# Performance work log

Hardware: AMD Instinct MI355X
Metric: run time of the kernel (lower is better)

## Reference

```python
import jax, jax.numpy as jnp
import numpy as np

N_HOPS = 3
N_NODES = 500000  # n_users + n_items


def setup_inputs() -> dict:
    key = jax.random.key(0)
    k1, k2, k3, k4, k5 = jax.random.split(key, 5)
    n_users, n_items, d, nnz = 100000, 400000, 64, 1250000
    return {
        "user_embed": jax.random.normal(k1, (n_users, d), dtype=jnp.float32),
        "item_embed": jax.random.normal(k2, (n_items, d), dtype=jnp.float32),
        "adj_row": jax.random.randint(k3, (nnz,), 0, n_users + n_items, dtype=jnp.int32),
        "adj_col": jax.random.randint(k4, (nnz,), 0, n_users + n_items, dtype=jnp.int32),
        "adj_val": jax.random.uniform(k5, (nnz,), dtype=jnp.float32),
        "n_users": n_users,
    }


def reference(user_embed, item_embed, adj_row, adj_col, adj_val, n_users):
    # all_embed: [N, d]
    all_embed = jnp.concatenate([user_embed, item_embed], axis=0)

    def spmm(x):
        # sparse @ dense: gather source-node features, scale by edge value,
        # scatter-add into destination rows. COO SpMM == SpecialSpmm.
        msgs = adj_val[:, None] * x[adj_col]          # [nnz, d]
        return jax.ops.segment_sum(msgs, adj_row, num_segments=N_NODES)

    agg = all_embed
    embs = [all_embed]
    for _ in range(N_HOPS):
        agg = spmm(agg)
        embs.append(agg)
    embs = jnp.stack(embs, axis=1)  # [N, n_hops+1, d]
    return embs[:n_users], embs[n_users:]
```

## Files before the change

### kernel.cpp

```cpp
#include <hip/hip_runtime.h>


#define DFEAT 64
#define ELLW 12

typedef float f32x4 __attribute__((ext_vector_type(4)));

__device__ inline unsigned bf16rne(float x) {
    unsigned u = __float_as_uint(x);
    u += 0x7FFF + ((u >> 16) & 1);
    return u;
}
__device__ inline unsigned pack2(float lo, float hi) {
    return (bf16rne(lo) >> 16) | (bf16rne(hi) & 0xFFFF0000u);
}
__device__ inline float bflo(unsigned w) { return __uint_as_float(w << 16); }
__device__ inline float bfhi(unsigned w) { return __uint_as_float(w & 0xFFFF0000u); }

__global__ void gc_zero(int4* __restrict__ p, int n4) {
    int i = blockIdx.x * blockDim.x + threadIdx.x;
    if (i < n4) p[i] = make_int4(0, 0, 0, 0);
}

__global__ void gc_fat(const float4* __restrict__ user4,
                       const float4* __restrict__ item4,
                       float4* __restrict__ out4, uint2* __restrict__ shadow0,
                       const int* __restrict__ row, const int* __restrict__ col,
                       const float* __restrict__ val,
                       int* __restrict__ cnt, float2* __restrict__ ell,
                       int* __restrict__ ovfcnt, int4* __restrict__ ovf,
                       int n_users, int n_nodes, int nnz, int initB) {
    int b = blockIdx.x;
    if (b < initB) {
        int tid = b * blockDim.x + threadIdx.x;
        if (tid >= n_nodes * 16) return;
        int node = tid >> 4;
        int q = tid & 15;
        float4 v = (node < n_users) ? user4[(size_t)node * 16 + q]
                                    : item4[(size_t)(node - n_users) * 16 + q];
        f32x4 nv = {v.x, v.y, v.z, v.w};
        __builtin_nontemporal_store(nv, (f32x4*)(out4 + (size_t)node * 64 + q));
        shadow0[(size_t)node * 16 + q] = make_uint2(pack2(v.x, v.y), pack2(v.z, v.w));
    } else {
        int i = (b - initB) * blockDim.x + threadIdx.x;
        if (i >= nnz) return;
        int r = row[i];
        int pos = atomicAdd(&cnt[r], 1);
        if (pos < ELLW) {
            ell[(size_t)r * ELLW + pos] = make_float2(__int_as_float(col[i] << 3), val[i]);
        } else {
            int o = atomicAdd(ovfcnt, 1);
            ovf[o] = make_int4(r, col[i] << 6, __float_as_int(val[i]), 0);
        }
    }
}

__global__ void gc_hop(const int* __restrict__ cnt,
                       const float4* __restrict__ ell4,
                       const int4* __restrict__ ssrc,
                       int4* __restrict__ sdst,
                       float* __restrict__ out, int hop, int n_nodes) {
    int tid = blockIdx.x * blockDim.x + threadIdx.x;
    int l = tid & 7;
    int r = tid >> 3;
    if (r >= n_nodes) return;
    int c = cnt[r];
    if (c > ELLW) c = ELLW;
    float4 a0 = make_float4(0.f, 0.f, 0.f, 0.f);
    float4 a1 = make_float4(0.f, 0.f, 0.f, 0.f);
    int e = 0;
    for (; e + 2 <= c; e += 2) {
        float4 s = ell4[(size_t)r * (ELLW / 2) + (e >> 1)];
        int i0 = __float_as_int(s.x) + l;
        int i1 = __float_as_int(s.z) + l;
        int4 g0 = ssrc[i0];
        int4 g1 = ssrc[i1];
        float v0 = s.y, v1 = s.w;
        a0.x += v0 * bflo(g0.x); a0.y += v0 * bfhi(g0.x);
        a0.z += v0 * bflo(g0.y); a0.w += v0 * bfhi(g0.y);
        a1.x += v0 * bflo(g0.z); a1.y += v0 * bfhi(g0.z);
        a1.z += v0 * bflo(g0.w); a1.w += v0 * bfhi(g0.w);
        a0.x += v1 * bflo(g1.x); a0.y += v1 * bfhi(g1.x);
        a0.z += v1 * bflo(g1.y); a0.w += v1 * bfhi(g1.y);
        a1.x += v1 * bflo(g1.z); a1.y += v1 * bfhi(g1.z);
        a1.z += v1 * bflo(g1.w); a1.w += v1 * bfhi(g1.w);
    }
    if (e < c) {
        float2 s = ((const float2*)ell4)[(size_t)r * ELLW + e];
        int i0 = __float_as_int(s.x) + l;
        int4 g0 = ssrc[i0];
        float v0 = s.y;
        a0.x += v0 * bflo(g0.x); a0.y += v0 * bfhi(g0.x);
        a0.z += v0 * bflo(g0.y); a0.w += v0 * bfhi(g0.y);
        a1.x += v0 * bflo(g0.z); a1.y += v0 * bfhi(g0.z);
        a1.z += v0 * bflo(g0.w); a1.w += v0 * bfhi(g0.w);
    }
    size_t dq = (size_t)r * 64 + (size_t)hop * 16 + l * 2;
    f32x4 n0 = {a0.x, a0.y, a0.z, a0.w};
    f32x4 n1 = {a1.x, a1.y, a1.z, a1.w};
    __builtin_nontemporal_store(n0, (f32x4*)((float4*)out) + dq);
    __builtin_nontemporal_store(n1, (f32x4*)((float4*)out) + dq + 1);
    if (sdst) {
        sdst[(size_t)r * 8 + l] = make_int4(pack2(a0.x, a0.y), pack2(a0.z, a0.w),
                                            pack2(a1.x, a1.y), pack2(a1.z, a1.w));
    }
}

__global__ void gc_ovf(const int* __restrict__ ovfcnt, const int4* __restrict__ ovf,
                       float* __restrict__ out, int hop) {
    int gtid = blockIdx.x * blockDim.x + threadIdx.x;
    int wave = gtid >> 6;
    int lane = gtid & 63;
    int nw = (gridDim.x * blockDim.x) >> 6;
    int cntv = *ovfcnt;
    size_t src_base = (size_t)(hop - 1) * 64 + lane;
    size_t dst_base = (size_t)hop * 64 + lane;
    for (int e = wave; e < cntv; e += nw) {
        int4 ed = ovf[e];
        float v = __int_as_float(ed.z);
        float x = out[(size_t)ed.y * 4 + src_base];
        unsafeAtomicAdd(&out[(size_t)ed.x * 256 + dst_base], v * x);
    }
}

__global__ void gc_sfix(const int* __restrict__ ovfcnt, const int4* __restrict__ ovf,
                        const float* __restrict__ out, unsigned short* __restrict__ shadow,
                        int hop) {
    int cntv = *ovfcnt;
    for (int i = blockIdx.x; i < cntv; i += gridDim.x) {
        int r = ovf[i].x;
        float x = out[(size_t)r * 256 + (size_t)hop * 64 + threadIdx.x];
        shadow[(size_t)r * 64 + threadIdx.x] = (unsigned short)(bf16rne(x) >> 16);
    }
}

__global__ void gc_init_out_full(const float4* __restrict__ user4,
                                 const float4* __restrict__ item4,
                                 float4* __restrict__ out4,
                                 int n_users, int n_nodes) {
    int tid = blockIdx.x * blockDim.x + threadIdx.x;
    if (tid >= n_nodes * 16) return;
    int node = tid >> 4;
    int q = tid & 15;
    float4 v = (node < n_users) ? user4[(size_t)node * 16 + q]
                                : item4[(size_t)(node - n_users) * 16 + q];
    float4 z = make_float4(0.f, 0.f, 0.f, 0.f);
    float4* p = out4 + (size_t)node * 64 + q;
    p[0] = v; p[16] = z; p[32] = z; p[48] = z;
}

__global__ void gc_spmm_atomic(const int* __restrict__ adj_row,
                               const int* __restrict__ adj_col,
                               const float* __restrict__ adj_val,
                               float* __restrict__ out, int hop, int nnz) {
    long long tid = (long long)blockIdx.x * blockDim.x + threadIdx.x;
    int e = (int)(tid >> 6);
    int j = (int)(tid & 63);
    if (e >= nnz) return;
    int r = adj_row[e];
    int c = adj_col[e];
    float v = adj_val[e];
    float x = out[(size_t)c * 256 + (size_t)(hop - 1) * 64 + j];
    unsafeAtomicAdd(&out[(size_t)r * 256 + (size_t)hop * 64 + j], v * x);
}

extern "C" void kernel_launch(void* const* d_in, const int* in_sizes, int n_in,
                              void* d_out, int out_size, void* d_ws, size_t ws_size,
                              hipStream_t stream) {
    const float* user_embed = (const float*)d_in[0];
    const float* item_embed = (const float*)d_in[1];
    const int*   adj_row    = (const int*)d_in[2];
    const int*   adj_col    = (const int*)d_in[3];
    const float* adj_val    = (const float*)d_in[4];
    const int n_users = in_sizes[0] / DFEAT;
    const int n_items = in_sizes[1] / DFEAT;
    const int n_nodes = n_users + n_items;
    const int nnz     = in_sizes[2];
    float* out = (float*)d_out;
    float4* out4 = (float4*)out;

    const int threads = 256;

    size_t off = 0;
    auto carve = [&](size_t bytes) { size_t o = off; off = (off + bytes + 255) & ~(size_t)255; return o; };
    size_t o_cnt    = carve((size_t)n_nodes * 4);
    size_t o_ovfcnt = carve(256);
    size_t zero_end = off;
    size_t o_ell    = carve((size_t)n_nodes * ELLW * 8);
    size_t o_ovf    = carve((size_t)nnz * 16);
    size_t o_shA    = carve((size_t)n_nodes * DFEAT * 2);
    size_t o_shB    = carve((size_t)n_nodes * DFEAT * 2);
    size_t needed = off;

    if (ws_size < needed) {
        int init_blocks = (n_nodes * 16 + threads - 1) / threads;
        hipLaunchKernelGGL(gc_init_out_full, dim3(init_blocks), dim3(threads), 0, stream,
                           (const float4*)user_embed, (const float4*)item_embed,
                           out4, n_users, n_nodes);
        long long spmm_total = (long long)nnz * 64;
        int spmm_blocks = (int)((spmm_total + threads - 1) / threads);
        for (int h = 1; h <= 3; ++h) {
            hipLaunchKernelGGL(gc_spmm_atomic, dim3(spmm_blocks), dim3(threads), 0, stream,
                               adj_row, adj_col, adj_val, out, h, nnz);
        }
        return;
    }

    char* ws = (char*)d_ws;
    int*    cnt    = (int*)(ws + o_cnt);
    int*    ovfcnt = (int*)(ws + o_ovfcnt);
    float2* ell    = (float2*)(ws + o_ell);
    int4*   ovf    = (int4*)(ws + o_ovf);
    char*   shA    = ws + o_shA;
    char*   shB    = ws + o_shB;

    int zn4 = (int)((zero_end - o_cnt) / 16);
    int zero_blocks = (zn4 + threads - 1) / threads;
    hipLaunchKernelGGL(gc_zero, dim3(zero_blocks), dim3(threads), 0, stream,
                       (int4*)(ws + o_cnt), zn4);

    int initB = (n_nodes * 16 + threads - 1) / threads;
    int scatB = (nnz + threads - 1) / threads;
    hipLaunchKernelGGL(gc_fat, dim3(initB + scatB), dim3(threads), 0, stream,
                       (const float4*)user_embed, (const float4*)item_embed,
                       out4, (uint2*)shA,
                       adj_row, adj_col, adj_val, cnt, ell, ovfcnt, ovf,
                       n_users, n_nodes, nnz, initB);

    long long hop_threads = (long long)n_nodes * 8;
    int hop_blocks = (int)((hop_threads + threads - 1) / threads);
    const int ovf_blocks = 256;
    char* scur = shA;
    char* snext = shB;
    for (int h = 1; h <= 3; ++h) {
        int4* sdst = (h < 3) ? (int4*)snext : (int4*)nullptr;
        hipLaunchKernelGGL(gc_hop, dim3(hop_blocks), dim3(threads), 0, stream,
                           cnt, (const float4*)ell, (const int4*)scur, sdst,
                           out, h, n_nodes);
        hipLaunchKernelGGL(gc_ovf, dim3(ovf_blocks), dim3(threads), 0, stream,
                           ovfcnt, ovf, out, h);
        if (h < 3) {
            hipLaunchKernelGGL(gc_sfix, dim3(256), dim3(64), 0, stream,
                               ovfcnt, ovf, out, (unsigned short*)snext, h);
            char* t = scur; scur = snext; snext = t;
        }
    }
}
```

Measured before the change: 326.6 us.

## Split bf16 shadow features into two planes and run hop per half

Stores the bf16 feature shadow as two planes of 32 features each and launches the hop kernel once per plane, with 4 threads per row instead of 8. Each launch gathers from a smaller random-access working set, which is meant to improve cache hit rates for the column gathers. In exchange, the ELL index and count arrays are read twice per hop and an extra launch is added.

```diff
diff --git a/kernel.cpp b/kernel.cpp
--- a/kernel.cpp
+++ b/kernel.cpp
@@ -24,7 +24,7 @@
 
 __global__ void gc_fat(const float4* __restrict__ user4,
                        const float4* __restrict__ item4,
-                       float4* __restrict__ out4, uint2* __restrict__ shadow0,
+                       float4* __restrict__ out4, char* __restrict__ shadow0,
                        const int* __restrict__ row, const int* __restrict__ col,
                        const float* __restrict__ val,
                        int* __restrict__ cnt, float2* __restrict__ ell,
@@ -40,14 +40,15 @@
                                     : item4[(size_t)(node - n_users) * 16 + q];
         f32x4 nv = {v.x, v.y, v.z, v.w};
         __builtin_nontemporal_store(nv, (f32x4*)(out4 + (size_t)node * 64 + q));
-        shadow0[(size_t)node * 16 + q] = make_uint2(pack2(v.x, v.y), pack2(v.z, v.w));
+        uint2* pl = (uint2*)(shadow0 + (size_t)(q >> 3) * n_nodes * 64);
+        pl[(size_t)node * 8 + (q & 7)] = make_uint2(pack2(v.x, v.y), pack2(v.z, v.w));
     } else {
         int i = (b - initB) * blockDim.x + threadIdx.x;
         if (i >= nnz) return;
         int r = row[i];
         int pos = atomicAdd(&cnt[r], 1);
         if (pos < ELLW) {
-            ell[(size_t)r * ELLW + pos] = make_float2(__int_as_float(col[i] << 3), val[i]);
+            ell[(size_t)r * ELLW + pos] = make_float2(__int_as_float(col[i] << 2), val[i]);
         } else {
             int o = atomicAdd(ovfcnt, 1);
             ovf[o] = make_int4(r, col[i] << 6, __float_as_int(val[i]), 0);
@@ -59,10 +60,10 @@
                        const float4* __restrict__ ell4,
                        const int4* __restrict__ ssrc,
                        int4* __restrict__ sdst,
-                       float* __restrict__ out, int hop, int n_nodes) {
+                       float* __restrict__ out, int hop, int fb, int n_nodes) {
     int tid = blockIdx.x * blockDim.x + threadIdx.x;
-    int l = tid & 7;
-    int r = tid >> 3;
+    int l = tid & 3;
+    int r = tid >> 2;
     if (r >= n_nodes) return;
     int c = cnt[r];
     if (c > ELLW) c = ELLW;
@@ -95,13 +96,13 @@
         a1.x += v0 * bflo(g0.z); a1.y += v0 * bfhi(g0.z);
         a1.z += v0 * bflo(g0.w); a1.w += v0 * bfhi(g0.w);
     }
-    size_t dq = (size_t)r * 64 + (size_t)hop * 16 + l * 2;
+    size_t dq = (size_t)r * 64 + (size_t)hop * 16 + fb * 8 + l * 2;
     f32x4 n0 = {a0.x, a0.y, a0.z, a0.w};
     f32x4 n1 = {a1.x, a1.y, a1.z, a1.w};
     __builtin_nontemporal_store(n0, (f32x4*)((float4*)out) + dq);
     __builtin_nontemporal_store(n1, (f32x4*)((float4*)out) + dq + 1);
     if (sdst) {
-        sdst[(size_t)r * 8 + l] = make_int4(pack2(a0.x, a0.y), pack2(a0.z, a0.w),
+        sdst[(size_t)r * 4 + l] = make_int4(pack2(a0.x, a0.y), pack2(a0.z, a0.w),
                                             pack2(a1.x, a1.y), pack2(a1.z, a1.w));
     }
 }
@@ -124,13 +125,15 @@
 }
 
 __global__ void gc_sfix(const int* __restrict__ ovfcnt, const int4* __restrict__ ovf,
-                        const float* __restrict__ out, unsigned short* __restrict__ shadow,
-                        int hop) {
+                        const float* __restrict__ out, char* __restrict__ shadow,
+                        int hop, int n_nodes) {
     int cntv = *ovfcnt;
+    int f = threadIdx.x;
+    unsigned short* pl = (unsigned short*)(shadow + (size_t)(f >> 5) * n_nodes * 64);
     for (int i = blockIdx.x; i < cntv; i += gridDim.x) {
         int r = ovf[i].x;
-        float x = out[(size_t)r * 256 + (size_t)hop * 64 + threadIdx.x];
-        shadow[(size_t)r * 64 + threadIdx.x] = (unsigned short)(bf16rne(x) >> 16);
+        float x = out[(size_t)r * 256 + (size_t)hop * 64 + f];
+        pl[(size_t)r * 32 + (f & 31)] = (unsigned short)(bf16rne(x) >> 16);
     }
 }
 
@@ -180,6 +183,7 @@
     float4* out4 = (float4*)out;
 
     const int threads = 256;
+    const size_t plane_bytes = (size_t)n_nodes * 64;
 
     size_t off = 0;
     auto carve = [&](size_t bytes) { size_t o = off; off = (off + bytes + 255) & ~(size_t)255; return o; };
@@ -188,8 +192,8 @@
     size_t zero_end = off;
     size_t o_ell    = carve((size_t)n_nodes * ELLW * 8);
     size_t o_ovf    = carve((size_t)nnz * 16);
-    size_t o_shA    = carve((size_t)n_nodes * DFEAT * 2);
-    size_t o_shB    = carve((size_t)n_nodes * DFEAT * 2);
+    size_t o_shA    = carve(plane_bytes * 2);
+    size_t o_shB    = carve(plane_bytes * 2);
     size_t needed = off;
 
     if (ws_size < needed) {
@@ -223,25 +227,29 @@
     int scatB = (nnz + threads - 1) / threads;
     hipLaunchKernelGGL(gc_fat, dim3(initB + scatB), dim3(threads), 0, stream,
                        (const float4*)user_embed, (const float4*)item_embed,
-                       out4, (uint2*)shA,
+                       out4, shA,
                        adj_row, adj_col, adj_val, cnt, ell, ovfcnt, ovf,
                        n_users, n_nodes, nnz, initB);
 
-    long long hop_threads = (long long)n_nodes * 8;
+    long long hop_threads = (long long)n_nodes * 4;
     int hop_blocks = (int)((hop_threads + threads - 1) / threads);
     const int ovf_blocks = 256;
     char* scur = shA;
     char* snext = shB;
     for (int h = 1; h <= 3; ++h) {
-        int4* sdst = (h < 3) ? (int4*)snext : (int4*)nullptr;
-        hipLaunchKernelGGL(gc_hop, dim3(hop_blocks), dim3(threads), 0, stream,
-                           cnt, (const float4*)ell, (const int4*)scur, sdst,
-                           out, h, n_nodes);
+        for (int fb = 0; fb < 2; ++fb) {
+            const int4* ssrc = (const int4*)(scur + (size_t)fb * plane_bytes);
+            int4* sdst = (h < 3) ? (int4*)(snext + (size_t)fb * plane_bytes)
+                                 : (int4*)nullptr;
+            hipLaunchKernelGGL(gc_hop, dim3(hop_blocks), dim3(threads), 0, stream,
+                               cnt, (const float4*)ell, ssrc, sdst,
+                               out, h, fb, n_nodes);
+        }
         hipLaunchKernelGGL(gc_ovf, dim3(ovf_blocks), dim3(threads), 0, stream,
                            ovfcnt, ovf, out, h);
         if (h < 3) {
             hipLaunchKernelGGL(gc_sfix, dim3(256), dim3(64), 0, stream,
-                               ovfcnt, ovf, out, (unsigned short*)snext, h);
+                               ovfcnt, ovf, out, snext, h, n_nodes);
             char* t = scur; scur = snext; snext = t;
         }
     }
```

Result: slower. 425.8 us (+30.4%).
